# Optimization experiments

Hardware: AMD Instinct MI355X
Metric: run time of the kernel (lower is better)

Reference implementation:

```python
import jax, jax.numpy as jnp
import numpy as np

N, E, DIN, DOUT, H = 50000, 800000, 256, 128, 8
DH = DOUT // H  # per-head dim = 16


def setup_inputs() -> dict:
    key = jax.random.key(0)
    k1, k2, k3, k4, k5 = jax.random.split(key, 5)
    x = jax.random.normal(k1, (N, DIN), dtype=jnp.float32)
    edge_index = jax.random.randint(k2, (2, E), 0, N)
    W_trans = jax.random.normal(k3, (DOUT, DIN), dtype=jnp.float32) / np.sqrt(DIN).astype(np.float32)
    W_att = jax.random.normal(k4, (1, 2 * DH), dtype=jnp.float32) / np.sqrt(2 * DH).astype(np.float32)
    b_att = jax.random.normal(k5, (1,), dtype=jnp.float32) * 0.01
    return {"x": x, "W_trans": W_trans, "W_att": W_att, "b_att": b_att, "edge_index": edge_index}


def reference(x, W_trans, W_att, b_att, edge_index):
    n = x.shape[0]
    # append self-loops (as in the torch module)
    loops = jnp.arange(n, dtype=edge_index.dtype)
    ei = jnp.concatenate([edge_index, jnp.stack([loops, loops])], axis=1)  # [2, E+N]
    src, dst = ei[0], ei[1]

    # linear transform, split heads: [n, H, DH]
    h = (x @ W_trans.T).reshape(n, H, DH)
    h_i = h[src]  # [Etot, H, DH]
    h_j = h[dst]  # [Etot, H, DH]

    # per-edge attention score: concat -> linear -> leaky_relu(0.2)
    s = jnp.concatenate([h_i, h_j], axis=-1) @ W_att.T + b_att  # [Etot, H, 1]
    s = jnp.where(s >= 0, s, 0.2 * s)

    # softmax(dim=0)*exp_sum/scatter_add(exp) == exp(s)/segment_sum(exp(s)) per dst node
    e = jnp.exp(s)
    denom = jax.ops.segment_sum(e, dst, num_segments=n)  # [n, H, 1]
    att = e / denom[dst]

    out = jax.ops.segment_sum(h_i * att, dst, num_segments=n)  # [n, H, DH]
    return out.reshape(n, DOUT)  # head_fusion='cat'
```

## Files before the change

### kernel.cpp

```cpp
#include <hip/hip_runtime.h>


constexpr int DIN  = 256;
constexpr int DOUT = 128;
constexpr int H    = 8;
constexpr int CAP  = 5120;
constexpr int CHUNK = 1024;

typedef __attribute__((ext_vector_type(8))) short bf16x8;
typedef __attribute__((ext_vector_type(4))) float f32x4;

__device__ __forceinline__ float lrelu(float s) { return s >= 0.0f ? s : 0.2f * s; }

__device__ __forceinline__ unsigned short f2bf(float f) {
  unsigned u = __float_as_uint(f);
  u += 0x7FFF + ((u >> 16) & 1);
  return (unsigned short)(u >> 16);
}
__device__ __forceinline__ float bflo(unsigned u) { return __uint_as_float(u << 16); }
__device__ __forceinline__ float bfhi(unsigned u) { return __uint_as_float(u & 0xFFFF0000u); }

__device__ __forceinline__ int wave_incl_scan(int v, int lane) {
#pragma unroll
  for (int d = 1; d < 64; d <<= 1) {
    int t = __shfl_up(v, d, 64);
    if (lane >= d) v += t;
  }
  return v;
}

__global__ void conv_w(const float* __restrict__ W, unsigned short* __restrict__ Wbf,
                       int n, int* __restrict__ bcount, int nb) {
  int i = blockIdx.x * blockDim.x + threadIdx.x;
  if (i < n) Wbf[i] = f2bf(W[i]);
  if (blockIdx.x == 0 && threadIdx.x < nb) bcount[threadIdx.x] = 0;
}

__global__ __launch_bounds__(256) void bp_gemm(const float* __restrict__ x,
                                               const unsigned short* __restrict__ Wbf,
                                               unsigned short* __restrict__ hbf, int N,
                                               const int* __restrict__ ei,
                                               int* __restrict__ bcount,
                                               unsigned* __restrict__ pair_buf,
                                               int E, int nb, int bp_blocks) {
  __shared__ int hist[256];
  __shared__ int gbase[256];
  if ((int)blockIdx.x < bp_blocks) {
    int c0 = blockIdx.x * CHUNK;
    hist[threadIdx.x] = 0;
    __syncthreads();
    int dcache[4];
#pragma unroll
    for (int q = 0; q < 4; ++q) {
      int e = c0 + q * 256 + threadIdx.x;
      dcache[q] = (e < E) ? ei[E + e] : -1;
      if (dcache[q] >= 0) atomicAdd(&hist[dcache[q] >> 8], 1);
    }
    __syncthreads();
    if (threadIdx.x < nb) {
      int c = hist[threadIdx.x];
      gbase[threadIdx.x] = c ? atomicAdd(&bcount[threadIdx.x], c) : 0;
    }
    __syncthreads();
    hist[threadIdx.x] = 0;
    __syncthreads();
#pragma unroll
    for (int q = 0; q < 4; ++q) {
      int e = c0 + q * 256 + threadIdx.x;
      if (dcache[q] >= 0) {
        int s = ei[e];
        int bk = dcache[q] >> 8;
        int r = atomicAdd(&hist[bk], 1);
        pair_buf[bk * CAP + gbase[bk] + r] = ((unsigned)s << 8) | (unsigned)(dcache[q] & 255);
      }
    }
    return;
  }
  int gb = blockIdx.x - bp_blocks;
  int tid = threadIdx.x;
  int w = tid >> 6, lane = tid & 63;
  int mr = lane & 15, kg = lane >> 4;
  int m0 = gb * 32 + (w >> 1) * 16;
  int nt0 = (w & 1) * 4;
  if (m0 >= N) return;
  int rr = m0 + mr;
  if (rr >= N) rr = N - 1;
  const float* xrow = x + (size_t)rr * DIN + kg * 8;

  float4 xa[8], xc[8];
#pragma unroll
  for (int ks = 0; ks < 8; ++ks) {
    xa[ks] = *(const float4*)(xrow + ks * 32);
    xc[ks] = *(const float4*)(xrow + ks * 32 + 4);
  }

  f32x4 acc[4];
#pragma unroll
  for (int t = 0; t < 4; ++t) acc[t] = (f32x4){0.f, 0.f, 0.f, 0.f};

#pragma unroll
  for (int ks = 0; ks < 8; ++ks) {
    bf16x8 a;
    a[0] = (short)f2bf(xa[ks].x); a[1] = (short)f2bf(xa[ks].y);
    a[2] = (short)f2bf(xa[ks].z); a[3] = (short)f2bf(xa[ks].w);
    a[4] = (short)f2bf(xc[ks].x); a[5] = (short)f2bf(xc[ks].y);
    a[6] = (short)f2bf(xc[ks].z); a[7] = (short)f2bf(xc[ks].w);
#pragma unroll
    for (int t = 0; t < 4; ++t) {
      bf16x8 b = *(const bf16x8*)(Wbf + ((nt0 + t) * 16 + mr) * DIN + ks * 32 + kg * 8);
      acc[t] = __builtin_amdgcn_mfma_f32_16x16x32_bf16(a, b, acc[t], 0, 0, 0);
    }
  }
#pragma unroll
  for (int t = 0; t < 4; ++t) {
#pragma unroll
    for (int r = 0; r < 4; ++r) {
      int row = m0 + kg * 4 + r;
      if (row < N) hbf[row * DOUT + (nt0 + t) * 16 + mr] = f2bf(acc[t][r]);
    }
  }
}

__global__ __launch_bounds__(256) void fs_ns(const unsigned* __restrict__ pair_buf,
                                             const int* __restrict__ bcount,
                                             int* __restrict__ offsets,
                                             unsigned short* __restrict__ src_sorted,
                                             const unsigned short* __restrict__ hbf,
                                             const float* __restrict__ Wa,
                                             float* __restrict__ a_src,
                                             float* __restrict__ a_dst,
                                             int N, int E, int nb) {
  __shared__ int cnt[256];
  __shared__ int cur[256];
  __shared__ int redS[256];
  __shared__ int wsumS[4];
  const int t = threadIdx.x;
  if ((int)blockIdx.x >= nb) {
    int idx = ((int)blockIdx.x - nb) * 256 + t;
    if (idx >= N * H) return;
    int v = idx >> 3, hh = idx & 7;
    const unsigned short* hp = hbf + (size_t)v * DOUT + hh * 16;
    uint4 p0 = *(const uint4*)hp;
    uint4 p1 = *(const uint4*)(hp + 8);
    float hv[16];
    hv[0] = bflo(p0.x); hv[1] = bfhi(p0.x); hv[2] = bflo(p0.y); hv[3] = bfhi(p0.y);
    hv[4] = bflo(p0.z); hv[5] = bfhi(p0.z); hv[6] = bflo(p0.w); hv[7] = bfhi(p0.w);
    hv[8] = bflo(p1.x); hv[9] = bfhi(p1.x); hv[10] = bflo(p1.y); hv[11] = bfhi(p1.y);
    hv[12] = bflo(p1.z); hv[13] = bfhi(p1.z); hv[14] = bflo(p1.w); hv[15] = bfhi(p1.w);
    float s1 = 0.f, s2 = 0.f;
#pragma unroll
    for (int d = 0; d < 16; ++d) {
      s1 += hv[d] * Wa[d];
      s2 += hv[d] * Wa[16 + d];
    }
    a_src[idx] = s1;
    a_dst[idx] = s2;
    return;
  }
  const int B = blockIdx.x;
  const int node0 = B * 256;
  const int v = node0 + t;
  const int valid = (v < N);
  cnt[t] = valid ? 1 : 0;
  __syncthreads();
  const int cntE = bcount[B];
  const unsigned* reg = pair_buf + B * CAP;
  for (int i = t; i < cntE; i += 256)
    atomicAdd(&cnt[reg[i] & 255], 1);
  redS[t] = (t < B) ? bcount[t] : 0;
  __syncthreads();
  for (int s = 128; s > 0; s >>= 1) {
    if (t < s) redS[t] += redS[t + s];
    __syncthreads();
  }
  const int csr_base = redS[0] + node0;
  int val = cnt[t];
  int lane = t & 63, wv = t >> 6;
  int inc = wave_incl_scan(val, lane);
  if (lane == 63) wsumS[wv] = inc;
  __syncthreads();
  int base = 0;
  for (int q = 0; q < wv; ++q) base += wsumS[q];
  int ex = base + inc - val;
  cur[t] = ex + 1;
  if (valid) {
    offsets[v] = csr_base + ex;
    src_sorted[csr_base + ex] = (unsigned short)v;
  }
  if (B == 0 && t == 0) offsets[N] = E + N;
  __syncthreads();
  for (int i = t; i < cntE; i += 256) {
    unsigned p = reg[i];
    int k = atomicAdd(&cur[p & 255], 1);
    src_sorted[csr_base + k] = (unsigned short)(p >> 8);
  }
}

__global__ __launch_bounds__(256) void aggregate(const unsigned short* __restrict__ hbf,
                                                 const float* __restrict__ a_src,
                                                 const float* __restrict__ a_dst,
                                                 const float* __restrict__ b_att,
                                                 const int* __restrict__ offsets,
                                                 const unsigned short* __restrict__ src_sorted,
                                                 float* __restrict__ out, int N) {
  int wid = blockIdx.x * 4 + (threadIdx.x >> 6);
  if (wid >= N) return;
  int lane = threadIdx.x & 63;
  int g = lane >> 4, sl = lane & 15;
  int head = sl >> 1;
  float adv = a_dst[wid * H + head] + b_att[0];
  int beg = offsets[wid], end = offsets[wid + 1];
  float a0 = 0, a1 = 0, a2 = 0, a3 = 0, a4 = 0, a5 = 0, a6 = 0, a7 = 0, den = 0;
  for (int j0 = beg; j0 < end; j0 += 4) {
    int jj = j0 + g;
    bool valid = jj < end;
    int jc = valid ? jj : beg;
    int s = src_sorted[jc];
    float as = a_src[s * H + head];
    uint4 u = *(const uint4*)(hbf + s * DOUT + sl * 8);
    float e = valid ? __expf(lrelu(as + adv)) : 0.f;
    den += e;
    a0 += e * bflo(u.x); a1 += e * bfhi(u.x);
    a2 += e * bflo(u.y); a3 += e * bfhi(u.y);
    a4 += e * bflo(u.z); a5 += e * bfhi(u.z);
    a6 += e * bflo(u.w); a7 += e * bfhi(u.w);
  }
  den += __shfl_xor(den, 16, 64); den += __shfl_xor(den, 32, 64);
  a0 += __shfl_xor(a0, 16, 64); a0 += __shfl_xor(a0, 32, 64);
  a1 += __shfl_xor(a1, 16, 64); a1 += __shfl_xor(a1, 32, 64);
  a2 += __shfl_xor(a2, 16, 64); a2 += __shfl_xor(a2, 32, 64);
  a3 += __shfl_xor(a3, 16, 64); a3 += __shfl_xor(a3, 32, 64);
  a4 += __shfl_xor(a4, 16, 64); a4 += __shfl_xor(a4, 32, 64);
  a5 += __shfl_xor(a5, 16, 64); a5 += __shfl_xor(a5, 32, 64);
  a6 += __shfl_xor(a6, 16, 64); a6 += __shfl_xor(a6, 32, 64);
  a7 += __shfl_xor(a7, 16, 64); a7 += __shfl_xor(a7, 32, 64);
  float inv = 1.0f / den;
  if (g == 0) {
    float4 o = make_float4(a0 * inv, a1 * inv, a2 * inv, a3 * inv);
    *(float4*)&out[wid * DOUT + sl * 8] = o;
  } else if (g == 1) {
    float4 o = make_float4(a4 * inv, a5 * inv, a6 * inv, a7 * inv);
    *(float4*)&out[wid * DOUT + sl * 8 + 4] = o;
  }
}

extern "C" void kernel_launch(void* const* d_in, const int* in_sizes, int n_in,
                              void* d_out, int out_size, void* d_ws, size_t ws_size,
                              hipStream_t stream) {
  const float* x     = (const float*)d_in[0];
  const float* W     = (const float*)d_in[1];
  const float* Wa    = (const float*)d_in[2];
  const float* b_att = (const float*)d_in[3];
  const int*   ei    = (const int*)d_in[4];
  const int N  = in_sizes[0] / DIN;
  const int E  = in_sizes[4] / 2;
  const int NB = (N + 255) / 256;
  float* out = (float*)d_out;

  char* p = (char*)d_ws;
  auto take = [&p](size_t bytes) {
    uintptr_t u = ((uintptr_t)p + 15) & ~(uintptr_t)15;
    p = (char*)(u + bytes);
    return (void*)u;
  };
  unsigned short* hbf = (unsigned short*)take((size_t)N * DOUT * 2);
  unsigned short* Wbf = (unsigned short*)take((size_t)DOUT * DIN * 2);
  float* a_src        = (float*)take((size_t)N * H * 4);
  float* a_dst        = (float*)take((size_t)N * H * 4);
  int* bcount         = (int*)take((size_t)NB * 4);
  unsigned* pair_buf  = (unsigned*)take((size_t)NB * CAP * 4);
  int* offsets        = (int*)take((size_t)(N + 1) * 4);
  unsigned short* src_sorted = (unsigned short*)take((size_t)(E + N + 16) * 2);

  dim3 b256(256);
  const int bp_blocks   = (E + CHUNK - 1) / CHUNK;
  const int gemm_blocks = (N + 31) / 32;
  const int ns_blocks   = (N * H + 255) / 256;

  conv_w<<<dim3((DOUT * DIN + 255) / 256), b256, 0, stream>>>(W, Wbf, DOUT * DIN, bcount, NB);
  bp_gemm<<<dim3(bp_blocks + gemm_blocks), b256, 0, stream>>>(
      x, Wbf, hbf, N, ei, bcount, pair_buf, E, NB, bp_blocks);
  fs_ns<<<dim3(NB + ns_blocks), b256, 0, stream>>>(
      pair_buf, bcount, offsets, src_sorted, hbf, Wa, a_src, a_dst, N, E, NB);
  aggregate<<<dim3((N + 3) / 4), b256, 0, stream>>>(hbf, a_src, a_dst, b_att, offsets,
                                                    src_sorted, out, N);
}
```

Before: 202.5 us.

## Enlarge bucket chunks, give each GEMM wave full output width, unroll aggregate by two

The binning phase now processes 4096 edges per block instead of 1024, which cuts block count and global atomics on the bucket counters. The GEMM is remapped so each wave computes a 16-row by 128-column tile, loading each x row once instead of twice, with 64 rows per block. The aggregation loop handles two edges per lane group per iteration to expose more memory-level parallelism. The costs are higher register pressure in the GEMM and binning phases and fewer binning blocks.

```diff
diff --git a/kernel.cpp b/kernel.cpp
--- a/kernel.cpp
+++ b/kernel.cpp
@@ -5,7 +5,7 @@
 constexpr int DOUT = 128;
 constexpr int H    = 8;
 constexpr int CAP  = 5120;
-constexpr int CHUNK = 1024;
+constexpr int CHUNK = 4096;
 
 typedef __attribute__((ext_vector_type(8))) short bf16x8;
 typedef __attribute__((ext_vector_type(4))) float f32x4;
@@ -49,9 +49,9 @@
     int c0 = blockIdx.x * CHUNK;
     hist[threadIdx.x] = 0;
     __syncthreads();
-    int dcache[4];
-#pragma unroll
-    for (int q = 0; q < 4; ++q) {
+    int dcache[16];
+#pragma unroll
+    for (int q = 0; q < 16; ++q) {
       int e = c0 + q * 256 + threadIdx.x;
       dcache[q] = (e < E) ? ei[E + e] : -1;
       if (dcache[q] >= 0) atomicAdd(&hist[dcache[q] >> 8], 1);
@@ -65,7 +65,7 @@
     hist[threadIdx.x] = 0;
     __syncthreads();
 #pragma unroll
-    for (int q = 0; q < 4; ++q) {
+    for (int q = 0; q < 16; ++q) {
       int e = c0 + q * 256 + threadIdx.x;
       if (dcache[q] >= 0) {
         int s = ei[e];
@@ -76,47 +76,41 @@
     }
     return;
   }
-  int gb = blockIdx.x - bp_blocks;
-  int tid = threadIdx.x;
-  int w = tid >> 6, lane = tid & 63;
-  int mr = lane & 15, kg = lane >> 4;
-  int m0 = gb * 32 + (w >> 1) * 16;
-  int nt0 = (w & 1) * 4;
+  int wid = (blockIdx.x - bp_blocks) * 4 + (threadIdx.x >> 6);
+  int m0 = wid * 16;
   if (m0 >= N) return;
+  int lane = threadIdx.x & 63;
+  int mr = lane & 15;
+  int kg = lane >> 4;
   int rr = m0 + mr;
   if (rr >= N) rr = N - 1;
   const float* xrow = x + (size_t)rr * DIN + kg * 8;
 
-  float4 xa[8], xc[8];
+  f32x4 acc[8];
+#pragma unroll
+  for (int t = 0; t < 8; ++t) acc[t] = (f32x4){0.f, 0.f, 0.f, 0.f};
+
 #pragma unroll
   for (int ks = 0; ks < 8; ++ks) {
-    xa[ks] = *(const float4*)(xrow + ks * 32);
-    xc[ks] = *(const float4*)(xrow + ks * 32 + 4);
-  }
-
-  f32x4 acc[4];
-#pragma unroll
-  for (int t = 0; t < 4; ++t) acc[t] = (f32x4){0.f, 0.f, 0.f, 0.f};
-
-#pragma unroll
-  for (int ks = 0; ks < 8; ++ks) {
+    float4 alo = *(const float4*)(xrow + ks * 32);
+    float4 ahi = *(const float4*)(xrow + ks * 32 + 4);
     bf16x8 a;
-    a[0] = (short)f2bf(xa[ks].x); a[1] = (short)f2bf(xa[ks].y);
-    a[2] = (short)f2bf(xa[ks].z); a[3] = (short)f2bf(xa[ks].w);
-    a[4] = (short)f2bf(xc[ks].x); a[5] = (short)f2bf(xc[ks].y);
-    a[6] = (short)f2bf(xc[ks].z); a[7] = (short)f2bf(xc[ks].w);
-#pragma unroll
-    for (int t = 0; t < 4; ++t) {
-      bf16x8 b = *(const bf16x8*)(Wbf + ((nt0 + t) * 16 + mr) * DIN + ks * 32 + kg * 8);
+    a[0] = (short)f2bf(alo.x); a[1] = (short)f2bf(alo.y);
+    a[2] = (short)f2bf(alo.z); a[3] = (short)f2bf(alo.w);
+    a[4] = (short)f2bf(ahi.x); a[5] = (short)f2bf(ahi.y);
+    a[6] = (short)f2bf(ahi.z); a[7] = (short)f2bf(ahi.w);
+#pragma unroll
+    for (int t = 0; t < 8; ++t) {
+      bf16x8 b = *(const bf16x8*)(Wbf + ((size_t)(t * 16 + mr) * DIN + ks * 32 + kg * 8));
       acc[t] = __builtin_amdgcn_mfma_f32_16x16x32_bf16(a, b, acc[t], 0, 0, 0);
     }
   }
 #pragma unroll
-  for (int t = 0; t < 4; ++t) {
+  for (int t = 0; t < 8; ++t) {
 #pragma unroll
     for (int r = 0; r < 4; ++r) {
       int row = m0 + kg * 4 + r;
-      if (row < N) hbf[row * DOUT + (nt0 + t) * 16 + mr] = f2bf(acc[t][r]);
+      if (row < N) hbf[(size_t)row * DOUT + t * 16 + mr] = f2bf(acc[t][r]);
     }
   }
 }
@@ -211,19 +205,26 @@
   float adv = a_dst[wid * H + head] + b_att[0];
   int beg = offsets[wid], end = offsets[wid + 1];
   float a0 = 0, a1 = 0, a2 = 0, a3 = 0, a4 = 0, a5 = 0, a6 = 0, a7 = 0, den = 0;
-  for (int j0 = beg; j0 < end; j0 += 4) {
-    int jj = j0 + g;
-    bool valid = jj < end;
-    int jc = valid ? jj : beg;
-    int s = src_sorted[jc];
-    float as = a_src[s * H + head];
-    uint4 u = *(const uint4*)(hbf + s * DOUT + sl * 8);
-    float e = valid ? __expf(lrelu(as + adv)) : 0.f;
-    den += e;
-    a0 += e * bflo(u.x); a1 += e * bfhi(u.x);
-    a2 += e * bflo(u.y); a3 += e * bfhi(u.y);
-    a4 += e * bflo(u.z); a5 += e * bfhi(u.z);
-    a6 += e * bflo(u.w); a7 += e * bfhi(u.w);
+  for (int j0 = beg; j0 < end; j0 += 8) {
+    int ja = j0 + g, jb = j0 + 4 + g;
+    bool va = ja < end, vb = jb < end;
+    int sa = src_sorted[va ? ja : beg];
+    int sb = src_sorted[vb ? jb : beg];
+    float asa = a_src[sa * H + head];
+    float asb = a_src[sb * H + head];
+    uint4 ua = *(const uint4*)(hbf + sa * DOUT + sl * 8);
+    uint4 ub = *(const uint4*)(hbf + sb * DOUT + sl * 8);
+    float ea = va ? __expf(lrelu(asa + adv)) : 0.f;
+    float eb = vb ? __expf(lrelu(asb + adv)) : 0.f;
+    den += ea + eb;
+    a0 += ea * bflo(ua.x) + eb * bflo(ub.x);
+    a1 += ea * bfhi(ua.x) + eb * bfhi(ub.x);
+    a2 += ea * bflo(ua.y) + eb * bflo(ub.y);
+    a3 += ea * bfhi(ua.y) + eb * bfhi(ub.y);
+    a4 += ea * bflo(ua.z) + eb * bflo(ub.z);
+    a5 += ea * bfhi(ua.z) + eb * bfhi(ub.z);
+    a6 += ea * bflo(ua.w) + eb * bflo(ub.w);
+    a7 += ea * bfhi(ua.w) + eb * bfhi(ub.w);
   }
   den += __shfl_xor(den, 16, 64); den += __shfl_xor(den, 32, 64);
   a0 += __shfl_xor(a0, 16, 64); a0 += __shfl_xor(a0, 32, 64);
@@ -274,7 +275,7 @@
 
   dim3 b256(256);
   const int bp_blocks   = (E + CHUNK - 1) / CHUNK;
-  const int gemm_blocks = (N + 31) / 32;
+  const int gemm_blocks = ((N + 15) / 16 + 3) / 4;
   const int ns_blocks   = (N * H + 255) / 256;
 
   conv_w<<<dim3((DOUT * DIN + 255) / 256), b256, 0, stream>>>(W, Wbf, DOUT * DIN, bcount, NB);
```

Result: faster. 185.0 us (-8.6%).
